# Performance work log

Measured on AMD Instinct MI355X. Metric: run time of the kernel, lower is better.

## Reference

```python
import jax, jax.numpy as jnp
import numpy as np

B, S, D = 2, 2048, 1024
H = 16
HD = D // H  # 64


def setup_inputs() -> dict:
    key = jax.random.key(0)
    ks = jax.random.split(key, 6)
    scale = 1.0 / np.sqrt(D)
    return {
        "x": jax.random.normal(ks[0], (B, S, D), dtype=jnp.float32),
        "W_q": jax.random.normal(ks[1], (D, D), dtype=jnp.float32) * scale,
        "W_k": jax.random.normal(ks[2], (D, D), dtype=jnp.float32) * scale,
        "W_v": jax.random.normal(ks[3], (D, D), dtype=jnp.float32) * scale,
        "W_o": jax.random.normal(ks[4], (D, D), dtype=jnp.float32) * scale,
        "b_o": jax.random.normal(ks[5], (D,), dtype=jnp.float32) * 0.01,
    }


def reference(x, W_q, W_k, W_v, W_o, b_o):
    # Projections (torch Linear applies x @ W.T; weights here stored as [out, in])
    q = jnp.einsum("bsd,ed->bse", x, W_q).reshape(B, S, H, HD)
    k = jnp.einsum("bsd,ed->bse", x, W_k).reshape(B, S, H, HD)
    v = jnp.einsum("bsd,ed->bse", x, W_v).reshape(B, S, H, HD)
    # scores: [B, H, S, S]
    scores = jnp.einsum("bqhd,bkhd->bhqk", q, k) / jnp.sqrt(jnp.float32(HD))
    attn = jax.nn.softmax(scores, axis=-1)
    # dropout is identity in eval mode
    out = jnp.einsum("bhqk,bkhd->bqhd", attn, v).reshape(B, S, D)
    return jnp.einsum("bsd,ed->bse", out, W_o) + b_o
```

## Files before the change

kernel.cpp:

```cpp
#include <hip/hip_runtime.h>
#include <hip/hip_bf16.h>

typedef __hip_bfloat16 bf16_t;
typedef __bf16 bf16x8 __attribute__((ext_vector_type(8)));
typedef __bf16 bf16x4 __attribute__((ext_vector_type(4)));
typedef short  s16x4  __attribute__((ext_vector_type(4)));
typedef float  f32x4  __attribute__((ext_vector_type(4)));

#define MFMA(a, b, c) __builtin_amdgcn_mfma_f32_16x16x32_bf16((a), (b), (c), 0, 0, 0)

__device__ __forceinline__ f32x4 mfma16(bf16x4 a, bf16x4 b, f32x4 c) {
#if __has_builtin(__builtin_amdgcn_mfma_f32_16x16x16_bf16)
  return __builtin_amdgcn_mfma_f32_16x16x16_bf16(a, b, c, 0, 0, 0);
#else
  return __builtin_amdgcn_mfma_f32_16x16x16bf16_1k(
      __builtin_bit_cast(s16x4, a), __builtin_bit_cast(s16x4, b), c, 0, 0, 0);
#endif
}

__device__ __forceinline__ bf16x8 ldg8(const bf16_t* p) {
  return *reinterpret_cast<const bf16x8*>(p);
}
__device__ __forceinline__ bf16x4 ldg4(const bf16_t* p) {
  return *reinterpret_cast<const bf16x4*>(p);
}
__device__ __forceinline__ void st8(bf16_t* p, bf16x8 v) {
  *reinterpret_cast<bf16x8*>(p) = v;
}
__device__ __forceinline__ void store_out(bf16_t* p, float v) { *p = __float2bfloat16(v); }
__device__ __forceinline__ void store_out(float* p, float v)  { *p = v; }

__device__ __forceinline__ void async16(const bf16_t* g, bf16_t* l) {
  __builtin_amdgcn_global_load_lds(
      (const __attribute__((address_space(1))) void*)g,
      (__attribute__((address_space(3))) void*)l, 16, 0, 0);
}

__global__ __launch_bounds__(256) void cvt_kernel(
    const float* __restrict__ x,  const float* __restrict__ Wq,
    const float* __restrict__ Wk, const float* __restrict__ Wv,
    const float* __restrict__ Wo,
    bf16_t* __restrict__ xb,  bf16_t* __restrict__ Wqb,
    bf16_t* __restrict__ Wkb, bf16_t* __restrict__ Wvb,
    bf16_t* __restrict__ Wob) {
  const int bid = blockIdx.x;
  const float* src; bf16_t* dst; size_t base;
  float scl = 1.0f;
  if (bid < 2048)      { src = x;  dst = xb;  base = (size_t)bid * 2048; }
  else if (bid < 2560) { src = Wq; dst = Wqb; base = (size_t)(bid - 2048) * 2048;
                         scl = 0.180336878f; }
  else if (bid < 3072) { src = Wk; dst = Wkb; base = (size_t)(bid - 2560) * 2048; }
  else if (bid < 3584) { src = Wv; dst = Wvb; base = (size_t)(bid - 3072) * 2048; }
  else                 { src = Wo; dst = Wob; base = (size_t)(bid - 3584) * 2048; }
  const size_t i0 = base + (size_t)threadIdx.x * 8;
  const float4 f0 = *reinterpret_cast<const float4*>(src + i0);
  const float4 f1 = *reinterpret_cast<const float4*>(src + i0 + 4);
  bf16x8 v;
  v[0] = (__bf16)(f0.x * scl); v[1] = (__bf16)(f0.y * scl);
  v[2] = (__bf16)(f0.z * scl); v[3] = (__bf16)(f0.w * scl);
  v[4] = (__bf16)(f1.x * scl); v[5] = (__bf16)(f1.y * scl);
  v[6] = (__bf16)(f1.z * scl); v[7] = (__bf16)(f1.w * scl);
  st8(dst + i0, v);
}

#define GK 1024

template <typename OutT, bool BIAS>
__device__ __forceinline__ void gemm_tile(
    const bf16_t* __restrict__ A, const bf16_t* __restrict__ B,
    OutT* __restrict__ C, const float* __restrict__ bias,
    int bm, int bn, int ldc, bf16_t* As, bf16_t* Bs) {
  const int tid  = threadIdx.x;
  const int lane = tid & 63;
  const int wave = tid >> 6;
  const int wm   = (wave & 1) << 6;
  const int wn   = (wave >> 1) << 6;
  const int lr   = lane & 15;
  const int lq   = lane >> 4;

  const int srow = tid >> 3;
  const int sx   = ((tid & 7) ^ (srow & 7)) << 3;

  const bf16_t* Ag = A + (size_t)(bm + srow) * GK + sx;
  const bf16_t* Bg = B + (size_t)(bn + srow) * GK + sx;
  bf16_t* Asw = As + wave * 512;
  bf16_t* Bsw = Bs + wave * 512;

  f32x4 acc[4][4];
#pragma unroll
  for (int i = 0; i < 4; ++i)
#pragma unroll
    for (int j = 0; j < 4; ++j) acc[i][j] = (f32x4){0.f, 0.f, 0.f, 0.f};

  for (int k0 = 0; k0 < GK; k0 += 64) {
    __syncthreads();
#pragma unroll
    for (int g = 0; g < 4; ++g) {
      async16(Ag + k0 + (size_t)(g * 32) * GK, Asw + g * 2048);
      async16(Bg + k0 + (size_t)(g * 32) * GK, Bsw + g * 2048);
    }
    __syncthreads();
#pragma unroll
    for (int ks = 0; ks < 2; ++ks) {
      bf16x8 af[4], bf[4];
      const int chs = ((ks * 4 + lq) ^ (lr & 7)) << 3;
#pragma unroll
      for (int i = 0; i < 4; ++i) {
        af[i] = ldg8(&As[(wm + i * 16 + lr) * 64 + chs]);
        bf[i] = ldg8(&Bs[(wn + i * 16 + lr) * 64 + chs]);
      }
#pragma unroll
      for (int mi = 0; mi < 4; ++mi)
#pragma unroll
        for (int ni = 0; ni < 4; ++ni)
          acc[mi][ni] = MFMA(af[mi], bf[ni], acc[mi][ni]);
    }
  }

#pragma unroll
  for (int ni = 0; ni < 4; ++ni) {
    const int col = bn + wn + ni * 16 + lr;
    float bv = 0.f;
    if (BIAS) bv = bias[col];
#pragma unroll
    for (int mi = 0; mi < 4; ++mi) {
#pragma unroll
      for (int r = 0; r < 4; ++r) {
        const int row = bm + wm + mi * 16 + lq * 4 + r;
        store_out(&C[(size_t)row * ldc + col], acc[mi][ni][r] + bv);
      }
    }
  }
}

__global__ __launch_bounds__(256) void qkv_kernel(
    const bf16_t* __restrict__ x, const bf16_t* __restrict__ Wq,
    const bf16_t* __restrict__ Wk, const bf16_t* __restrict__ Wv,
    bf16_t* __restrict__ Q, bf16_t* __restrict__ Kp, bf16_t* __restrict__ Vt) {
  __shared__ alignas(16) bf16_t As[128 * 64];
  __shared__ alignas(16) bf16_t Bs[128 * 64];
  const int bid = blockIdx.x;
  const int z   = blockIdx.y;
  const int mt  = (bid & 31) * 128;
  const int nt  = (bid >> 5) * 128;
  if (z == 0) {
    gemm_tile<bf16_t, false>(x, Wq, Q, nullptr, mt, nt, 1024, As, Bs);
  } else if (z == 1) {
    gemm_tile<bf16_t, false>(x, Wk, Kp, nullptr, mt, nt, 1024, As, Bs);
  } else {
    gemm_tile<bf16_t, false>(Wv, x, Vt, nullptr, nt, mt, 4096, As, Bs);
  }
}

__global__ __launch_bounds__(256) void out_proj_kernel(
    const bf16_t* __restrict__ Ao, const bf16_t* __restrict__ Wo,
    const float* __restrict__ bias, float* __restrict__ out) {
  __shared__ alignas(16) bf16_t As[128 * 64];
  __shared__ alignas(16) bf16_t Bs[128 * 64];
  const int bid = blockIdx.x;
  gemm_tile<float, true>(Ao, Wo, out, bias, (bid & 31) * 128, (bid >> 5) * 128, 1024, As, Bs);
}

#define VPAD 68

__global__ __launch_bounds__(256) void attn_kernel(
    const bf16_t* __restrict__ Q, const bf16_t* __restrict__ Kp,
    const bf16_t* __restrict__ Vt, bf16_t* __restrict__ Ao) {
  __shared__ alignas(16) bf16_t Ks[64 * 64];
  __shared__ alignas(16) bf16_t Vs[64 * VPAD];
  __shared__ float Osc[4][64 * 17];

  const int tid  = threadIdx.x;
  const int lane = tid & 63;
  const int wave = tid >> 6;
  const int lr   = lane & 15;
  const int lq   = lane >> 4;
  const int bh   = blockIdx.x;
  const int qt   = blockIdx.y;
  const int b    = bh >> 4;
  const int h    = bh & 15;
  const size_t tok0 = (size_t)b * 2048;
  const int col0 = h * 64;

  const size_t qrow = tok0 + qt * 64 + wave * 16 + lr;
  bf16x8 qf[2];
  qf[0] = ldg8(&Q[qrow * 1024 + col0 + lq * 8]);
  qf[1] = ldg8(&Q[qrow * 1024 + col0 + 32 + lq * 8]);

  f32x4 o[4];
#pragma unroll
  for (int i = 0; i < 4; ++i) o[i] = (f32x4){0.f, 0.f, 0.f, 0.f};
  float lsum = 0.f;

  const int srow = tid >> 3;
  const int sxk  = ((tid & 7) ^ (srow & 7)) << 3;
  const int sxv  = (tid & 7) << 3;
  bf16_t* Ksw = Ks + wave * 512;

  const int koff0 = lr * 64 + ((lq ^ (lr & 7)) << 3);
  const int koff1 = lr * 64 + (((lq + 4) ^ (lr & 7)) << 3);
  const int voff  = lr * VPAD + lq * 4;

  for (int kv0 = 0; kv0 < 2048; kv0 += 64) {
    const bf16_t* Kg = Kp + (tok0 + kv0) * 1024 + col0;
    const bf16_t* Vg = Vt + (size_t)col0 * 4096 + tok0 + kv0;
    const bf16x8 v0 = ldg8(Vg + (size_t)srow * 4096 + sxv);
    const bf16x8 v1 = ldg8(Vg + (size_t)(srow + 32) * 4096 + sxv);
    __syncthreads();
    async16(Kg + (size_t)srow * 1024 + sxk, Ksw);
    async16(Kg + (size_t)(srow + 32) * 1024 + sxk, Ksw + 2048);
    st8(&Vs[srow * VPAD + sxv], v0);
    st8(&Vs[(srow + 32) * VPAD + sxv], v1);
    __syncthreads();

#pragma unroll
    for (int c = 0; c < 4; ++c) {
      const bf16x8 kf0 = ldg8(&Ks[c * 1024 + koff0]);
      const bf16x8 kf1 = ldg8(&Ks[c * 1024 + koff1]);
      f32x4 sT = {0.f, 0.f, 0.f, 0.f};
      sT = MFMA(kf0, qf[0], sT);
      sT = MFMA(kf1, qf[1], sT);
      const float p0 = exp2f(sT.x);
      const float p1 = exp2f(sT.y);
      const float p2 = exp2f(sT.z);
      const float p3 = exp2f(sT.w);
      bf16x4 pb;
      pb[0] = (__bf16)p0; pb[1] = (__bf16)p1;
      pb[2] = (__bf16)p2; pb[3] = (__bf16)p3;
      lsum += (p0 + p1) + (p2 + p3);
#pragma unroll
      for (int ht = 0; ht < 4; ++ht) {
        const bf16x4 vf = ldg4(&Vs[ht * 16 * VPAD + voff + c * 16]);
        o[ht] = mfma16(vf, pb, o[ht]);
      }
    }
  }

  lsum += __shfl_xor(lsum, 16);
  lsum += __shfl_xor(lsum, 32);
  const float invl = 1.f / lsum;

  float* Ow = &Osc[wave][0];
#pragma unroll
  for (int ht = 0; ht < 4; ++ht)
#pragma unroll
    for (int r = 0; r < 4; ++r)
      Ow[(ht * 16 + lq * 4 + r) * 17 + lr] = o[ht][r] * invl;

  const int qq = lane >> 2;
  const int hc = (lane & 3) * 16;
  bf16x8 w0, w1;
#pragma unroll
  for (int i = 0; i < 8; ++i) {
    w0[i] = (__bf16)Ow[(hc + i) * 17 + qq];
    w1[i] = (__bf16)Ow[(hc + 8 + i) * 17 + qq];
  }
  bf16_t* dst = Ao + (tok0 + qt * 64 + wave * 16 + qq) * 1024 + col0 + hc;
  st8(dst, w0);
  st8(dst + 8, w1);
}

extern "C" void kernel_launch(void* const* d_in, const int* in_sizes, int n_in,
                              void* d_out, int out_size, void* d_ws, size_t ws_size,
                              hipStream_t stream) {
  const float* x  = (const float*)d_in[0];
  const float* Wq = (const float*)d_in[1];
  const float* Wk = (const float*)d_in[2];
  const float* Wv = (const float*)d_in[3];
  const float* Wo = (const float*)d_in[4];
  const float* bo = (const float*)d_in[5];
  float* out = (float*)d_out;

  const size_t NTOK = 4096, DMODEL = 1024, WSZ = DMODEL * DMODEL;
  bf16_t* xb  = (bf16_t*)d_ws;
  bf16_t* Wqb = xb + NTOK * DMODEL;
  bf16_t* Wkb = Wqb + WSZ;
  bf16_t* Wvb = Wkb + WSZ;
  bf16_t* Wob = Wvb + WSZ;
  bf16_t* Q   = Wob + WSZ;
  bf16_t* Kp  = Q  + NTOK * DMODEL;
  bf16_t* Vt  = Kp + NTOK * DMODEL;
  bf16_t* Ao  = Vt + NTOK * DMODEL;

  cvt_kernel<<<dim3(4096), 256, 0, stream>>>(x, Wq, Wk, Wv, Wo, xb, Wqb, Wkb, Wvb, Wob);
  qkv_kernel<<<dim3(256, 3), 256, 0, stream>>>(xb, Wqb, Wkb, Wvb, Q, Kp, Vt);
  attn_kernel<<<dim3(32, 32), 256, 0, stream>>>(Q, Kp, Vt, Ao);
  out_proj_kernel<<<dim3(256, 1), 256, 0, stream>>>(Ao, Wob, bo, out);
}
```

Before: 217.9 us.

## Process two query tiles per wave in attention to reuse K/V loads

Each wave in the attention kernel now handles 32 query rows as two 16-row subtiles. Each K/V tile staged into shared memory therefore feeds twice as many MFMAs, and the grid's query dimension is halved. Shared memory for Ks/Vs and the output scratch is aliased into one buffer, with a barrier before the epilogue, to keep LDS usage low. The trade-off is higher register pressure and only 512 blocks, which may reduce occupancy and latency hiding.

Measured after the change: 209.2 us. 4.0% less time.

```diff
diff --git a/kernel.cpp b/kernel.cpp
--- a/kernel.cpp
+++ b/kernel.cpp
@@ -166,9 +166,10 @@
 __global__ __launch_bounds__(256) void attn_kernel(
     const bf16_t* __restrict__ Q, const bf16_t* __restrict__ Kp,
     const bf16_t* __restrict__ Vt, bf16_t* __restrict__ Ao) {
-  __shared__ alignas(16) bf16_t Ks[64 * 64];
-  __shared__ alignas(16) bf16_t Vs[64 * VPAD];
-  __shared__ float Osc[4][64 * 17];
+  __shared__ alignas(16) char smem_raw[4 * 64 * 17 * 4];
+  bf16_t* Ks = (bf16_t*)smem_raw;
+  bf16_t* Vs = (bf16_t*)(smem_raw + 8192);
+  float*  Osc = (float*)smem_raw;
 
   const int tid  = threadIdx.x;
   const int lane = tid & 63;
@@ -181,16 +182,23 @@
   const int h    = bh & 15;
   const size_t tok0 = (size_t)b * 2048;
   const int col0 = h * 64;
-
-  const size_t qrow = tok0 + qt * 64 + wave * 16 + lr;
-  bf16x8 qf[2];
-  qf[0] = ldg8(&Q[qrow * 1024 + col0 + lq * 8]);
-  qf[1] = ldg8(&Q[qrow * 1024 + col0 + 32 + lq * 8]);
-
-  f32x4 o[4];
-#pragma unroll
-  for (int i = 0; i < 4; ++i) o[i] = (f32x4){0.f, 0.f, 0.f, 0.f};
-  float lsum = 0.f;
+  const int qblk = qt * 128 + wave * 32;
+
+  bf16x8 qf[2][2];
+#pragma unroll
+  for (int nt = 0; nt < 2; ++nt) {
+    const size_t qrow = tok0 + qblk + nt * 16 + lr;
+#pragma unroll
+    for (int c = 0; c < 2; ++c)
+      qf[nt][c] = ldg8(&Q[qrow * 1024 + col0 + c * 32 + lq * 8]);
+  }
+
+  f32x4 o[2][4];
+#pragma unroll
+  for (int nt = 0; nt < 2; ++nt)
+#pragma unroll
+    for (int i = 0; i < 4; ++i) o[nt][i] = (f32x4){0.f, 0.f, 0.f, 0.f};
+  float lsum[2] = {0.f, 0.f};
 
   const int srow = tid >> 3;
   const int sxk  = ((tid & 7) ^ (srow & 7)) << 3;
@@ -217,47 +225,57 @@
     for (int c = 0; c < 4; ++c) {
       const bf16x8 kf0 = ldg8(&Ks[c * 1024 + koff0]);
       const bf16x8 kf1 = ldg8(&Ks[c * 1024 + koff1]);
-      f32x4 sT = {0.f, 0.f, 0.f, 0.f};
-      sT = MFMA(kf0, qf[0], sT);
-      sT = MFMA(kf1, qf[1], sT);
-      const float p0 = exp2f(sT.x);
-      const float p1 = exp2f(sT.y);
-      const float p2 = exp2f(sT.z);
-      const float p3 = exp2f(sT.w);
-      bf16x4 pb;
-      pb[0] = (__bf16)p0; pb[1] = (__bf16)p1;
-      pb[2] = (__bf16)p2; pb[3] = (__bf16)p3;
-      lsum += (p0 + p1) + (p2 + p3);
+      bf16x4 pb[2];
+#pragma unroll
+      for (int nt = 0; nt < 2; ++nt) {
+        f32x4 sT = {0.f, 0.f, 0.f, 0.f};
+        sT = MFMA(kf0, qf[nt][0], sT);
+        sT = MFMA(kf1, qf[nt][1], sT);
+        const float p0 = exp2f(sT.x);
+        const float p1 = exp2f(sT.y);
+        const float p2 = exp2f(sT.z);
+        const float p3 = exp2f(sT.w);
+        pb[nt][0] = (__bf16)p0; pb[nt][1] = (__bf16)p1;
+        pb[nt][2] = (__bf16)p2; pb[nt][3] = (__bf16)p3;
+        lsum[nt] += (p0 + p1) + (p2 + p3);
+      }
 #pragma unroll
       for (int ht = 0; ht < 4; ++ht) {
         const bf16x4 vf = ldg4(&Vs[ht * 16 * VPAD + voff + c * 16]);
-        o[ht] = mfma16(vf, pb, o[ht]);
+        o[0][ht] = mfma16(vf, pb[0], o[0][ht]);
+        o[1][ht] = mfma16(vf, pb[1], o[1][ht]);
       }
     }
   }
 
-  lsum += __shfl_xor(lsum, 16);
-  lsum += __shfl_xor(lsum, 32);
-  const float invl = 1.f / lsum;
-
-  float* Ow = &Osc[wave][0];
-#pragma unroll
-  for (int ht = 0; ht < 4; ++ht)
-#pragma unroll
-    for (int r = 0; r < 4; ++r)
-      Ow[(ht * 16 + lq * 4 + r) * 17 + lr] = o[ht][r] * invl;
-
-  const int qq = lane >> 2;
-  const int hc = (lane & 3) * 16;
-  bf16x8 w0, w1;
-#pragma unroll
-  for (int i = 0; i < 8; ++i) {
-    w0[i] = (__bf16)Ow[(hc + i) * 17 + qq];
-    w1[i] = (__bf16)Ow[(hc + 8 + i) * 17 + qq];
-  }
-  bf16_t* dst = Ao + (tok0 + qt * 64 + wave * 16 + qq) * 1024 + col0 + hc;
-  st8(dst, w0);
-  st8(dst + 8, w1);
+  __syncthreads();
+
+  float* Ow = &Osc[wave * 64 * 17];
+#pragma unroll
+  for (int nt = 0; nt < 2; ++nt) {
+    float ls = lsum[nt];
+    ls += __shfl_xor(ls, 16);
+    ls += __shfl_xor(ls, 32);
+    const float invl = 1.f / ls;
+
+#pragma unroll
+    for (int ht = 0; ht < 4; ++ht)
+#pragma unroll
+      for (int r = 0; r < 4; ++r)
+        Ow[(ht * 16 + lq * 4 + r) * 17 + lr] = o[nt][ht][r] * invl;
+
+    const int qq = lane >> 2;
+    const int hc = (lane & 3) * 16;
+    bf16x8 w0, w1;
+#pragma unroll
+    for (int i = 0; i < 8; ++i) {
+      w0[i] = (__bf16)Ow[(hc + i) * 17 + qq];
+      w1[i] = (__bf16)Ow[(hc + 8 + i) * 17 + qq];
+    }
+    bf16_t* dst = Ao + (tok0 + qblk + nt * 16 + qq) * 1024 + col0 + hc;
+    st8(dst, w0);
+    st8(dst + 8, w1);
+  }
 }
 
 extern "C" void kernel_launch(void* const* d_in, const int* in_sizes, int n_in,
@@ -284,6 +302,6 @@
 
   cvt_kernel<<<dim3(4096), 256, 0, stream>>>(x, Wq, Wk, Wv, Wo, xb, Wqb, Wkb, Wvb, Wob);
   qkv_kernel<<<dim3(256, 3), 256, 0, stream>>>(xb, Wqb, Wkb, Wvb, Q, Kp, Vt);
-  attn_kernel<<<dim3(32, 32), 256, 0, stream>>>(Q, Kp, Vt, Ao);
+  attn_kernel<<<dim3(32, 16), 256, 0, stream>>>(Q, Kp, Vt, Ao);
   out_proj_kernel<<<dim3(256, 1), 256, 0, stream>>>(Ao, Wob, bo, out);
 }
```
